# Performance work log

Measured on AMD Instinct MI355X. Metric: run time of the kernel, lower is better.

## Reference

```python
import jax, jax.numpy as jnp
import numpy as np

LN_EPS = 1e-5


def setup_inputs() -> dict:
    key = jax.random.key(0)
    ks = jax.random.split(key, 14)
    b, T, C = 1, 1024, 192
    ATTN, CONT, F = 4, 2, 8  # attn_dims, content_dims, conv feature channels
    s = 0.05
    H = jax.random.normal(ks[0], (b, C, T), jnp.float32)
    d = jax.random.randint(ks[1], (b, T), 2, 8)            # durations in [2,8)
    src_mask = jnp.ones((b, 1, T), dtype=bool)             # True = valid token
    return {
        "H": H, "d": d, "src_mask": src_mask,
        # proj_in: Linear(C,C) + SiLU
        "W_in": jax.random.normal(ks[2], (C, C)) * s, "b_in": jnp.zeros((C,)),
        # ConvLN: Conv1d(C->8, k=3, pad=1) + LayerNorm(8)
        "conv_w": jax.random.normal(ks[3], (F, C, 3)) * s, "conv_b": jnp.zeros((F,)),
        "gamma": jnp.ones((F,)), "beta": jnp.zeros((F,)),
        # W_proj: Linear(10,10)+SiLU+Linear(10,4)+softmax(dim=t_text)
        "wp1": jax.random.normal(ks[4], (10, 10)) * s, "bp1": jnp.zeros((10,)),
        "wp2": jax.random.normal(ks[5], (10, ATTN)) * s, "bp2": jnp.zeros((ATTN,)),
        # C_proj: Linear(10,10)+SiLU+Linear(10,2)+SiLU
        "wc1": jax.random.normal(ks[6], (10, 10)) * s, "bc1": jnp.zeros((10,)),
        "wc2": jax.random.normal(ks[7], (10, CONT)) * s, "bc2": jnp.zeros((CONT,)),
        # proj_WH: Linear(4*C, C); proj_WC: Linear(4*2, C)
        "W_WH": jax.random.normal(ks[8], (ATTN * C, C)) * s, "b_WH": jnp.zeros((C,)),
        "W_WC": jax.random.normal(ks[9], (ATTN * CONT, C)) * s, "b_WC": jnp.zeros((C,)),
        # proj_out: Conv1d(C, C, 1) == pointwise linear over channels
        "W_out": jax.random.normal(ks[10], (C, C)) * s, "b_out": jnp.zeros((C,)),
    }


def reference(H, d, src_mask, W_in, b_in, conv_w, conv_b, gamma, beta,
              wp1, bp1, wp2, bp2, wc1, bc1, wc2, bc2,
              W_WH, b_WH, W_WC, b_WC, W_out, b_out):
    b, C, T = H.shape
    df = d.astype(jnp.float32)
    mel_len = jnp.sum(d, axis=1)                                  # [b]
    t_mel = int(jnp.max(mel_len))                                 # static from concrete d
    frame_valid = jnp.arange(t_mel)[None, :] < mel_len[:, None]   # [b,M] True=valid frame
    tbm = (src_mask[:, 0, None, :] & frame_valid[:, :, None]).astype(jnp.float32)  # [b,M,T]

    # token boundary grid: S = frame_idx - start, E = end - frame_idx
    i = jnp.arange(1, t_mel + 1, dtype=jnp.float32)[None, :, None]  # [1,M,1]
    E_d = jnp.cumsum(df, axis=1)[:, None, :]                        # [b,1,T] token ends
    S_d = E_d - df[:, None, :]                                      # [b,1,T] token starts
    S = (i - S_d) * tbm                                             # [b,M,T]
    E = (E_d - i) * tbm                                             # [b,M,T]

    # proj_in (on [b,T,C]) then ConvLN(C->8) + SiLU
    x = jax.nn.silu(jnp.einsum('bct,cd->btd', H, W_in) + b_in)      # [b,T,C]
    xc = jax.lax.conv_general_dilated(
        jnp.transpose(x, (0, 2, 1)), conv_w, (1,), [(1, 1)],
        dimension_numbers=('NCH', 'OIH', 'NCH')) + conv_b[None, :, None]  # [b,8,T]
    xt = jnp.transpose(xc, (0, 2, 1))                               # [b,T,8]
    mu = jnp.mean(xt, axis=-1, keepdims=True)
    var = jnp.mean(jnp.square(xt - mu), axis=-1, keepdims=True)
    xt = (xt - mu) * jax.lax.rsqrt(var + LN_EPS) * gamma + beta
    xf = jax.nn.silu(xt)                                            # [b,T,8]

    # broadcast conv features over mel frames, cat with S/E boundary scalars
    feats = jnp.concatenate(
        [S[..., None], E[..., None],
         jnp.broadcast_to(xf[:, None, :, :], (b, t_mel, T, xf.shape[-1]))],
        axis=-1)                                                    # [b,M,T,10]

    # W_proj: tiny MLP + softmax over t_text
    W_att = jax.nn.softmax(jax.nn.silu(feats @ wp1 + bp1) @ wp2 + bp2, axis=2)  # [b,M,T,4]
    # C_proj: tiny MLP with SiLU output
    Cm = jax.nn.silu(jax.nn.silu(feats @ wc1 + bc1) @ wc2 + bc2)    # [b,M,T,2]

    WC = jnp.einsum('bmtq,bmtp->bmqp', W_att, Cm).reshape(b, t_mel, -1)  # [b,M,8]
    WH = jnp.einsum('bmtq,bht->bmqh', W_att, H).reshape(b, t_mel, -1)    # [b,M,768]
    O = (WC @ W_WC + b_WC) + (WH @ W_WH + b_WH)                     # [b,M,C]
    O = O @ W_out + b_out                                           # proj_out (1x1 conv)
    O = jnp.transpose(O, (0, 2, 1)) * frame_valid[:, None, :].astype(O.dtype)  # [b,C,M]
    return O, ~frame_valid
```

## Files before the change

### kernel.cpp

```cpp
#include <hip/hip_runtime.h>
#include <math.h>

#define T 1024
#define C 192
#define LN_EPS 1e-5f

typedef __attribute__((ext_vector_type(4))) float f32x4;
typedef __attribute__((ext_vector_type(8))) __bf16 bf16x8;

__device__ __forceinline__ float silu_f(float x){
    return x * __builtin_amdgcn_rcpf(1.0f + __expf(-x));
}
__device__ __forceinline__ float wred_max(float v){
    #pragma unroll
    for(int o=32;o;o>>=1) v = fmaxf(v, __shfl_xor(v,o));
    return v;
}
__device__ __forceinline__ float wred_sum(float v){
    #pragma unroll
    for(int o=32;o;o>>=1) v += __shfl_xor(v,o);
    return v;
}

__global__ void k_scan(const int* __restrict__ d, float* __restrict__ Sd, float* __restrict__ Ed){
    __shared__ int s[T];
    int tid = threadIdx.x;
    int v = d[tid];
    s[tid] = v;
    for(int off=1; off<T; off<<=1){
        __syncthreads();
        int add = (tid>=off) ? s[tid-off] : 0;
        __syncthreads();
        s[tid] += add;
    }
    __syncthreads();
    Ed[tid] = (float)s[tid];
    Sd[tid] = (float)(s[tid]-v);
}

__global__ void k_proj_in(const float* __restrict__ H, const float* __restrict__ W_in,
                          const float* __restrict__ b_in, float* __restrict__ x){
    __shared__ float Hs[192*4];
    int tid = threadIdx.x;
    int t0 = blockIdx.x*4;
    for(int idx=tid; idx<768; idx+=192){
        int ci = idx>>2, j = idx&3;
        Hs[idx] = H[ci*T + t0 + j];
    }
    __syncthreads();
    int c = tid;
    float acc[4];
    float bb = b_in[c];
    #pragma unroll
    for(int j=0;j<4;j++) acc[j] = bb;
    for(int ci=0; ci<192; ci++){
        float wv = W_in[ci*C + c];
        float4 h4 = *(const float4*)&Hs[ci*4];
        acc[0] += h4.x*wv; acc[1] += h4.y*wv;
        acc[2] += h4.z*wv; acc[3] += h4.w*wv;
    }
    #pragma unroll
    for(int j=0;j<4;j++) x[(t0+j)*C + c] = silu_f(acc[j]);
}

__global__ void k_conv_ln(const float* __restrict__ x, const float* __restrict__ conv_w,
                          const float* __restrict__ conv_b, const float* __restrict__ gamma,
                          const float* __restrict__ beta, float* __restrict__ xf){
    __shared__ float part[16][8][2];
    __shared__ float xcv[16][8];
    int tid = threadIdx.x;
    int cc = tid & 1, f = (tid>>1)&7, tl = tid>>4;
    int t = blockIdx.x*16 + tl;
    float acc = 0.f;
    for(int k=0;k<3;k++){
        int tt = t + k - 1;
        if(tt>=0 && tt<T){
            const float* xr = x + tt*C + cc*96;
            const float* wr = conv_w + f*C*3 + k + cc*96*3;
            for(int c2=0;c2<96;c2++) acc += xr[c2]*wr[c2*3];
        }
    }
    part[tl][f][cc] = acc;
    __syncthreads();
    if(cc==0){
        xcv[tl][f] = part[tl][f][0] + part[tl][f][1] + conv_b[f];
    }
    __syncthreads();
    if(cc==0){
        float a = xcv[tl][f];
        float mu=0.f;
        #pragma unroll
        for(int j=0;j<8;j++) mu += xcv[tl][j];
        mu *= 0.125f;
        float var=0.f;
        #pragma unroll
        for(int j=0;j<8;j++){ float dd = xcv[tl][j]-mu; var += dd*dd; }
        var *= 0.125f;
        float vi = rsqrtf(var + LN_EPS);
        float v = (a - mu)*vi*gamma[f] + beta[f];
        xf[t*8+f] = silu_f(v);
    }
}

__global__ void k_A(const float* __restrict__ Sd, const float* __restrict__ Ed,
                    const float* __restrict__ xf,
                    const float* __restrict__ wp1, const float* __restrict__ bp1,
                    const float* __restrict__ wc1, const float* __restrict__ bc1,
                    float* __restrict__ A1, float* __restrict__ A2, float* __restrict__ uv){
    int b = blockIdx.x, tid = threadIdx.x;
    if(b==4){
        if(tid<10){
            uv[tid]    = wp1[tid] - wp1[10+tid];
            uv[10+tid] = wc1[tid] - wc1[10+tid];
        }
        return;
    }
    int t = b*256 + tid;
    float sd = Sd[t], ed = Ed[t];
    float xv[8];
    #pragma unroll
    for(int k=0;k<8;k++) xv[k] = xf[t*8+k];
    #pragma unroll
    for(int j=0;j<10;j++){
        float a1 = bp1[j] - sd*wp1[j] + ed*wp1[10+j];
        float a2 = bc1[j] - sd*wc1[j] + ed*wc1[10+j];
        #pragma unroll
        for(int k=0;k<8;k++){
            a1 += xv[k]*wp1[(2+k)*10+j];
            a2 += xv[k]*wc1[(2+k)*10+j];
        }
        A1[t*12+j] = a1;
        A2[t*12+j] = a2;
    }
    A1[t*12+10]=0.f; A1[t*12+11]=0.f;
    A2[t*12+10]=0.f; A2[t*12+11]=0.f;
}

__global__ void k_hb(const float* __restrict__ H, __bf16* __restrict__ Hb){
    int base = (blockIdx.x*256 + threadIdx.x)*8;
    float4 a = *(const float4*)(H + base);
    float4 b = *(const float4*)(H + base + 4);
    bf16x8 o;
    o[0]=(__bf16)a.x; o[1]=(__bf16)a.y; o[2]=(__bf16)a.z; o[3]=(__bf16)a.w;
    o[4]=(__bf16)b.x; o[5]=(__bf16)b.y; o[6]=(__bf16)b.z; o[7]=(__bf16)b.w;
    *(bf16x8*)(Hb + base) = o;
}

__global__ void k_fold(const float* __restrict__ W_WH, const float* __restrict__ W_WC,
                       const float* __restrict__ b_WH, const float* __restrict__ b_WC,
                       const float* __restrict__ W_out, const float* __restrict__ b_out,
                       __bf16* __restrict__ WfT, float* __restrict__ b2){
    int i = blockIdx.x, c = threadIdx.x;
    if(i < 768){
        float a = 0.f;
        for(int j=0;j<C;j++) a += W_WH[i*C+j]*W_out[j*C+c];
        WfT[c*800 + i] = (__bf16)a;
    } else if(i < 776){
        int r = i-768;
        float a = 0.f;
        for(int j=0;j<C;j++) a += W_WC[r*C+j]*W_out[j*C+c];
        WfT[c*800 + 768 + r] = (__bf16)a;
    } else if(i == 776){
        float a = b_out[c];
        for(int j=0;j<C;j++) a += (b_WH[j]+b_WC[j])*W_out[j*C+c];
        b2[c] = a;
    } else {
        for(int k=c; k<192*24; k+=192){
            int cc = k/24, j = k - (k/24)*24;
            WfT[cc*800 + 776 + j] = (__bf16)0.f;
        }
    }
}

__global__ void __launch_bounds__(256) __attribute__((amdgpu_waves_per_eu(4,4)))
k_main(const __bf16* __restrict__ Hb, const float* __restrict__ A1, const float* __restrict__ A2,
       const float* __restrict__ uv,
       const float* __restrict__ wp2, const float* __restrict__ bp2,
       const float* __restrict__ wc2, const float* __restrict__ bc2,
       const __bf16* __restrict__ WfT, const float* __restrict__ b2g,
       float* __restrict__ out, int M)
{
    __shared__ __align__(16) unsigned char smem[40960];
    __bf16* PTlb = (__bf16*)smem;
    __bf16* wT   = (__bf16*)(smem + 6656);
    float*  scr  = (float*)(smem + 6656 + 32768);
    float*  wsm  = scr + 288;

    int tid = threadIdx.x;
    int w = tid >> 6, lane = tid & 63;
    int m0 = blockIdx.x*4;

    if(tid < 40)      wsm[tid] = wp2[tid];
    else if(tid < 44) wsm[tid] = bp2[tid-40];
    else if(tid < 64) wsm[tid] = wc2[tid-44];
    else if(tid < 66) wsm[tid] = bc2[tid-64];
    else if(tid < 86) wsm[tid] = uv[tid-66];
    if(tid < 224){
        int mi = tid/56, k = 776 + tid - (tid/56)*56;
        PTlb[mi*832 + (k ^ (mi<<4))] = (__bf16)0.f;
    }
    __syncthreads();

    for(int mi=0; mi<4; mi++){
        float fi = (float)(m0 + 1 + mi);
        float l[4][4];
        #pragma unroll 1
        for(int ti=0; ti<4; ti++){
            int t = tid + ti*256;
            float4 a0 = *(const float4*)(A1 + t*12);
            float4 a1 = *(const float4*)(A1 + t*12 + 4);
            float4 a2v = *(const float4*)(A1 + t*12 + 8);
            float Av[10] = {a0.x,a0.y,a0.z,a0.w,a1.x,a1.y,a1.z,a1.w,a2v.x,a2v.y};
            float l0=wsm[40], l1=wsm[41], l2=wsm[42], l3=wsm[43];
            #pragma unroll
            for(int j=0;j<10;j++){
                float h = silu_f(Av[j] + fi*wsm[66+j]);
                l0 += h*wsm[j*4+0]; l1 += h*wsm[j*4+1];
                l2 += h*wsm[j*4+2]; l3 += h*wsm[j*4+3];
            }
            l[ti][0]=l0; l[ti][1]=l1; l[ti][2]=l2; l[ti][3]=l3;
        }
        #pragma unroll
        for(int q=0;q<4;q++){
            float lm = fmaxf(fmaxf(l[0][q],l[1][q]), fmaxf(l[2][q],l[3][q]));
            lm = wred_max(lm);
            if(lane==0) scr[mi*16 + w*4 + q] = lm;
        }
        __syncthreads();
        float mxq[4];
        #pragma unroll
        for(int q=0;q<4;q++){
            float a = fmaxf(scr[mi*16+0*4+q], scr[mi*16+1*4+q]);
            float b = fmaxf(scr[mi*16+2*4+q], scr[mi*16+3*4+q]);
            mxq[q] = fmaxf(a,b);
        }
        float sp4[4] = {0.f,0.f,0.f,0.f};
        #pragma unroll
        for(int ti=0;ti<4;ti++){
            int t = tid + ti*256;
            #pragma unroll
            for(int q=0;q<4;q++){
                float e = __expf(l[ti][q] - mxq[q]);
                l[ti][q] = e;
                int row = mi*4+q;
                wT[row*1024 + (t ^ ((row&7)<<3))] = (__bf16)e;
                sp4[q] += e;
            }
        }
        float wcp2[4][2];
        #pragma unroll
        for(int q=0;q<4;q++){ wcp2[q][0]=0.f; wcp2[q][1]=0.f; }
        #pragma unroll 1
        for(int ti=0;ti<4;ti++){
            int t = tid + ti*256;
            float4 b0 = *(const float4*)(A2 + t*12);
            float4 b1 = *(const float4*)(A2 + t*12 + 4);
            float4 b2v = *(const float4*)(A2 + t*12 + 8);
            float Bv[10] = {b0.x,b0.y,b0.z,b0.w,b1.x,b1.y,b1.z,b1.w,b2v.x,b2v.y};
            float g1c0 = wsm[64], g1c1 = wsm[65];
            #pragma unroll
            for(int j=0;j<10;j++){
                float g = silu_f(Bv[j] + fi*wsm[76+j]);
                g1c0 += g*wsm[44 + j*2 + 0];
                g1c1 += g*wsm[44 + j*2 + 1];
            }
            float c0 = silu_f(g1c0), c1 = silu_f(g1c1);
            #pragma unroll
            for(int q=0;q<4;q++){
                wcp2[q][0] += l[ti][q]*c0;
                wcp2[q][1] += l[ti][q]*c1;
            }
        }
        #pragma unroll
        for(int q=0;q<4;q++){
            sp4[q] = wred_sum(sp4[q]);
            wcp2[q][0] = wred_sum(wcp2[q][0]);
            wcp2[q][1] = wred_sum(wcp2[q][1]);
        }
        if(lane==0){
            int base = 64 + mi*48 + w*12;
            #pragma unroll
            for(int q=0;q<4;q++){
                scr[base + q] = sp4[q];
                scr[base + 4 + q*2 + 0] = wcp2[q][0];
                scr[base + 4 + q*2 + 1] = wcp2[q][1];
            }
        }
    }
    __syncthreads();

    if(tid < 16){
        int mi = tid>>2, q = tid&3;
        float s = scr[64+mi*48+0*12+q] + scr[64+mi*48+1*12+q]
                + scr[64+mi*48+2*12+q] + scr[64+mi*48+3*12+q];
        scr[256+tid] = 1.0f/s;
    }
    if(tid >= 32 && tid < 64){
        int j = tid - 32;
        int mi = j>>3, qp = j&7, q = qp>>1, p = qp&1;
        float num = scr[64+mi*48+0*12+4+q*2+p] + scr[64+mi*48+1*12+4+q*2+p]
                  + scr[64+mi*48+2*12+4+q*2+p] + scr[64+mi*48+3*12+4+q*2+p];
        float den = scr[64+mi*48+0*12+q] + scr[64+mi*48+1*12+q]
                  + scr[64+mi*48+2*12+q] + scr[64+mi*48+3*12+q];
        PTlb[mi*832 + ((768+qp) ^ (mi<<4))] = (__bf16)(num/den);
    }
    __syncthreads();

    int cl = lane & 15, kg = lane >> 4;
    int swzW = (cl&7)<<3;
    f32x4 acc1[3];
    #pragma unroll
    for(int i=0;i<3;i++) acc1[i] = (f32x4){0.f,0.f,0.f,0.f};
    const __bf16* Aptr = Hb + (size_t)(w*48 + cl)*1024 + kg*8;
    const __bf16* wTrow = wT + cl*1024;
    #pragma unroll 2
    for(int ks=0; ks<32; ks++){
        int k0 = ks*32;
        bf16x8 bf = *(const bf16x8*)&wTrow[(k0 + kg*8) ^ swzW];
        #pragma unroll
        for(int i=0;i<3;i++){
            bf16x8 af = *(const bf16x8*)(Aptr + i*16*1024 + k0);
            acc1[i] = __builtin_amdgcn_mfma_f32_16x16x32_bf16(af, bf, acc1[i], 0, 0, 0);
        }
    }
    {
        int mP = cl >> 2, qP = cl & 3;
        float invv = scr[256 + cl];
        int swzP = mP<<4;
        #pragma unroll
        for(int i=0;i<3;i++){
            int hb = w*48 + i*16 + kg*4;
            #pragma unroll
            for(int r=0;r<4;r++){
                int k = qP*192 + hb + r;
                PTlb[mP*832 + (k ^ swzP)] = (__bf16)(acc1[i][r] * invv);
            }
        }
    }
    __syncthreads();

    f32x4 acc2[3];
    #pragma unroll
    for(int i=0;i<3;i++) acc2[i] = (f32x4){0.f,0.f,0.f,0.f};
    const __bf16* A2ptr = WfT + (size_t)(w*48 + cl)*800 + kg*8;
    const __bf16* Prow = PTlb + cl*832;
    int swzP2 = (cl&3)<<4;
    #pragma unroll 2
    for(int ks=0; ks<25; ks++){
        int k0 = ks*32;
        bf16x8 bf = *(const bf16x8*)&Prow[(k0 + kg*8) ^ swzP2];
        #pragma unroll
        for(int i=0;i<3;i++){
            bf16x8 af = *(const bf16x8*)(A2ptr + i*16*800 + k0);
            acc2[i] = __builtin_amdgcn_mfma_f32_16x16x32_bf16(af, bf, acc2[i], 0, 0, 0);
        }
    }
    if(cl < 4 && m0 + cl < M){
        #pragma unroll
        for(int i=0;i<3;i++){
            int cb = w*48 + i*16 + kg*4;
            #pragma unroll
            for(int r=0;r<4;r++){
                out[(size_t)(cb+r)*M + m0 + cl] = acc2[i][r] + b2g[cb+r];
            }
        }
    }
    if(tid < 4 && m0 + tid < M) out[(size_t)C*M + m0 + tid] = 0.f;
}

extern "C" void kernel_launch(void* const* d_in, const int* in_sizes, int n_in,
                              void* d_out, int out_size, void* d_ws, size_t ws_size,
                              hipStream_t stream)
{
    const float* H      = (const float*)d_in[0];
    const int*   d      = (const int*)  d_in[1];
    const float* W_in   = (const float*)d_in[3];
    const float* b_in   = (const float*)d_in[4];
    const float* conv_w = (const float*)d_in[5];
    const float* conv_b = (const float*)d_in[6];
    const float* gamma  = (const float*)d_in[7];
    const float* beta   = (const float*)d_in[8];
    const float* wp1    = (const float*)d_in[9];
    const float* bp1    = (const float*)d_in[10];
    const float* wp2    = (const float*)d_in[11];
    const float* bp2    = (const float*)d_in[12];
    const float* wc1    = (const float*)d_in[13];
    const float* bc1    = (const float*)d_in[14];
    const float* wc2    = (const float*)d_in[15];
    const float* bc2    = (const float*)d_in[16];
    const float* W_WH   = (const float*)d_in[17];
    const float* b_WH   = (const float*)d_in[18];
    const float* W_WC   = (const float*)d_in[19];
    const float* b_WC   = (const float*)d_in[20];
    const float* W_out  = (const float*)d_in[21];
    const float* b_out  = (const float*)d_in[22];

    float* out = (float*)d_out;
    int M = out_size / 193;

    float* ws   = (float*)d_ws;
    float* Sd   = ws;
    float* Ed   = ws + 1024;
    float* A1   = ws + 2048;
    float* A2   = ws + 14336;
    float* uvp  = ws + 26624;
    float* b2   = ws + 26656;
    __bf16* WfT = (__bf16*)(ws + 26848);
    __bf16* Hb  = (__bf16*)(ws + 103648);
    float* x    = ws + 201952;
    float* xf   = ws + 398560;

    hipLaunchKernelGGL(k_scan,    dim3(1),   dim3(1024), 0, stream, d, Sd, Ed);
    hipLaunchKernelGGL(k_proj_in, dim3(256), dim3(192),  0, stream, H, W_in, b_in, x);
    hipLaunchKernelGGL(k_conv_ln, dim3(64),  dim3(256),  0, stream, x, conv_w, conv_b, gamma, beta, xf);
    hipLaunchKernelGGL(k_A,       dim3(5),   dim3(256),  0, stream, Sd, Ed, xf, wp1, bp1, wc1, bc1, A1, A2, uvp);
    hipLaunchKernelGGL(k_hb,      dim3(96),  dim3(256),  0, stream, H, Hb);
    hipLaunchKernelGGL(k_fold,    dim3(778), dim3(192),  0, stream, W_WH, W_WC, b_WH, b_WC, W_out, b_out, WfT, b2);
    hipLaunchKernelGGL(k_main,    dim3((M+3)/4), dim3(256), 0, stream,
                       Hb, A1, A2, uvp, wp2, bp2, wc2, bc2, WfT, b2, out, M);
}
```

Baseline: 192.2 us.

## Move softmax weight tile from LDS to global scratch and merge prep kernels

```diff
diff --git a/kernel.cpp b/kernel.cpp
--- a/kernel.cpp
+++ b/kernel.cpp
@@ -136,21 +136,25 @@
     A2[t*12+10]=0.f; A2[t*12+11]=0.f;
 }
 
-__global__ void k_hb(const float* __restrict__ H, __bf16* __restrict__ Hb){
-    int base = (blockIdx.x*256 + threadIdx.x)*8;
-    float4 a = *(const float4*)(H + base);
-    float4 b = *(const float4*)(H + base + 4);
-    bf16x8 o;
-    o[0]=(__bf16)a.x; o[1]=(__bf16)a.y; o[2]=(__bf16)a.z; o[3]=(__bf16)a.w;
-    o[4]=(__bf16)b.x; o[5]=(__bf16)b.y; o[6]=(__bf16)b.z; o[7]=(__bf16)b.w;
-    *(bf16x8*)(Hb + base) = o;
-}
-
-__global__ void k_fold(const float* __restrict__ W_WH, const float* __restrict__ W_WC,
+__global__ void k_prep(const float* __restrict__ W_WH, const float* __restrict__ W_WC,
                        const float* __restrict__ b_WH, const float* __restrict__ b_WC,
                        const float* __restrict__ W_out, const float* __restrict__ b_out,
-                       __bf16* __restrict__ WfT, float* __restrict__ b2){
-    int i = blockIdx.x, c = threadIdx.x;
+                       const float* __restrict__ H,
+                       __bf16* __restrict__ WfT, float* __restrict__ b2,
+                       __bf16* __restrict__ Hb){
+    int bid = blockIdx.x, tid = threadIdx.x;
+    if(bid >= 778){
+        int base = ((bid-778)*256 + tid)*8;
+        float4 a = *(const float4*)(H + base);
+        float4 b = *(const float4*)(H + base + 4);
+        bf16x8 o;
+        o[0]=(__bf16)a.x; o[1]=(__bf16)a.y; o[2]=(__bf16)a.z; o[3]=(__bf16)a.w;
+        o[4]=(__bf16)b.x; o[5]=(__bf16)b.y; o[6]=(__bf16)b.z; o[7]=(__bf16)b.w;
+        *(bf16x8*)(Hb + base) = o;
+        return;
+    }
+    int i = bid, c = tid;
+    if(c >= 192) return;
     if(i < 768){
         float a = 0.f;
         for(int j=0;j<C;j++) a += W_WH[i*C+j]*W_out[j*C+c];
@@ -172,23 +176,23 @@
     }
 }
 
-__global__ void __launch_bounds__(256) __attribute__((amdgpu_waves_per_eu(4,4)))
+__global__ void __launch_bounds__(256) __attribute__((amdgpu_waves_per_eu(6,8)))
 k_main(const __bf16* __restrict__ Hb, const float* __restrict__ A1, const float* __restrict__ A2,
        const float* __restrict__ uv,
        const float* __restrict__ wp2, const float* __restrict__ bp2,
        const float* __restrict__ wc2, const float* __restrict__ bc2,
        const __bf16* __restrict__ WfT, const float* __restrict__ b2g,
+       __bf16* __restrict__ Eg,
        float* __restrict__ out, int M)
 {
-    __shared__ __align__(16) unsigned char smem[40960];
-    __bf16* PTlb = (__bf16*)smem;
-    __bf16* wT   = (__bf16*)(smem + 6656);
-    float*  scr  = (float*)(smem + 6656 + 32768);
-    float*  wsm  = scr + 288;
+    __shared__ __align__(16) __bf16 PTlb[4*832];
+    __shared__ float scr[288];
+    __shared__ float wsm[96];
 
     int tid = threadIdx.x;
     int w = tid >> 6, lane = tid & 63;
     int m0 = blockIdx.x*4;
+    __bf16* Eblk = Eg + (size_t)m0*4096;
 
     if(tid < 40)      wsm[tid] = wp2[tid];
     else if(tid < 44) wsm[tid] = bp2[tid-40];
@@ -196,8 +200,8 @@
     else if(tid < 66) wsm[tid] = bc2[tid-64];
     else if(tid < 86) wsm[tid] = uv[tid-66];
     if(tid < 224){
-        int mi = tid/56, k = 776 + tid - (tid/56)*56;
-        PTlb[mi*832 + (k ^ (mi<<4))] = (__bf16)0.f;
+        int fb = tid/56, k = 776 + (tid - (tid/56)*56);
+        PTlb[fb*832 + (k ^ (fb<<3))] = (__bf16)0.f;
     }
     __syncthreads();
 
@@ -235,6 +239,7 @@
             mxq[q] = fmaxf(a,b);
         }
         float sp4[4] = {0.f,0.f,0.f,0.f};
+        __bf16* Erow = Eblk + mi*4096;
         #pragma unroll
         for(int ti=0;ti<4;ti++){
             int t = tid + ti*256;
@@ -242,8 +247,7 @@
             for(int q=0;q<4;q++){
                 float e = __expf(l[ti][q] - mxq[q]);
                 l[ti][q] = e;
-                int row = mi*4+q;
-                wT[row*1024 + (t ^ ((row&7)<<3))] = (__bf16)e;
+                Erow[q*1024 + t] = (__bf16)e;
                 sp4[q] += e;
             }
         }
@@ -302,21 +306,20 @@
                   + scr[64+mi*48+2*12+4+q*2+p] + scr[64+mi*48+3*12+4+q*2+p];
         float den = scr[64+mi*48+0*12+q] + scr[64+mi*48+1*12+q]
                   + scr[64+mi*48+2*12+q] + scr[64+mi*48+3*12+q];
-        PTlb[mi*832 + ((768+qp) ^ (mi<<4))] = (__bf16)(num/den);
+        PTlb[mi*832 + ((768+qp) ^ (mi<<3))] = (__bf16)(num/den);
     }
     __syncthreads();
 
     int cl = lane & 15, kg = lane >> 4;
-    int swzW = (cl&7)<<3;
     f32x4 acc1[3];
     #pragma unroll
     for(int i=0;i<3;i++) acc1[i] = (f32x4){0.f,0.f,0.f,0.f};
     const __bf16* Aptr = Hb + (size_t)(w*48 + cl)*1024 + kg*8;
-    const __bf16* wTrow = wT + cl*1024;
+    const __bf16* Bp   = Eblk + cl*1024 + kg*8;
     #pragma unroll 2
     for(int ks=0; ks<32; ks++){
         int k0 = ks*32;
-        bf16x8 bf = *(const bf16x8*)&wTrow[(k0 + kg*8) ^ swzW];
+        bf16x8 bf = *(const bf16x8*)(Bp + k0);
         #pragma unroll
         for(int i=0;i<3;i++){
             bf16x8 af = *(const bf16x8*)(Aptr + i*16*1024 + k0);
@@ -324,16 +327,16 @@
         }
     }
     {
-        int mP = cl >> 2, qP = cl & 3;
+        int fb = cl >> 2, qP = cl & 3;
         float invv = scr[256 + cl];
-        int swzP = mP<<4;
+        int swz = fb<<3;
         #pragma unroll
         for(int i=0;i<3;i++){
             int hb = w*48 + i*16 + kg*4;
             #pragma unroll
             for(int r=0;r<4;r++){
                 int k = qP*192 + hb + r;
-                PTlb[mP*832 + (k ^ swzP)] = (__bf16)(acc1[i][r] * invv);
+                PTlb[fb*832 + (k ^ swz)] = (__bf16)(acc1[i][r] * invv);
             }
         }
     }
@@ -342,17 +345,16 @@
     f32x4 acc2[3];
     #pragma unroll
     for(int i=0;i<3;i++) acc2[i] = (f32x4){0.f,0.f,0.f,0.f};
-    const __bf16* A2ptr = WfT + (size_t)(w*48 + cl)*800 + kg*8;
-    const __bf16* Prow = PTlb + cl*832;
-    int swzP2 = (cl&3)<<4;
+    const __bf16* A2p = WfT + (size_t)(w*48 + cl)*800 + kg*8;
+    int prow = (cl&3)*832, swz2 = (cl&3)<<3;
     #pragma unroll 2
     for(int ks=0; ks<25; ks++){
         int k0 = ks*32;
-        bf16x8 bf = *(const bf16x8*)&Prow[(k0 + kg*8) ^ swzP2];
+        bf16x8 bb = *(const bf16x8*)&PTlb[prow + ((k0 + kg*8) ^ swz2)];
         #pragma unroll
         for(int i=0;i<3;i++){
-            bf16x8 af = *(const bf16x8*)(A2ptr + i*16*800 + k0);
-            acc2[i] = __builtin_amdgcn_mfma_f32_16x16x32_bf16(af, bf, acc2[i], 0, 0, 0);
+            bf16x8 af = *(const bf16x8*)(A2p + i*16*800 + k0);
+            acc2[i] = __builtin_amdgcn_mfma_f32_16x16x32_bf16(af, bb, acc2[i], 0, 0, 0);
         }
     }
     if(cl < 4 && m0 + cl < M){
@@ -397,6 +399,7 @@
 
     float* out = (float*)d_out;
     int M = out_size / 193;
+    int Mcap = ((M+3)/4)*4;
 
     float* ws   = (float*)d_ws;
     float* Sd   = ws;
@@ -409,13 +412,14 @@
     __bf16* Hb  = (__bf16*)(ws + 103648);
     float* x    = ws + 201952;
     float* xf   = ws + 398560;
+    __bf16* Eg  = (__bf16*)(ws + 406752);
 
     hipLaunchKernelGGL(k_scan,    dim3(1),   dim3(1024), 0, stream, d, Sd, Ed);
+    hipLaunchKernelGGL(k_prep,    dim3(874), dim3(256),  0, stream,
+                       W_WH, W_WC, b_WH, b_WC, W_out, b_out, H, WfT, b2, Hb);
     hipLaunchKernelGGL(k_proj_in, dim3(256), dim3(192),  0, stream, H, W_in, b_in, x);
     hipLaunchKernelGGL(k_conv_ln, dim3(64),  dim3(256),  0, stream, x, conv_w, conv_b, gamma, beta, xf);
     hipLaunchKernelGGL(k_A,       dim3(5),   dim3(256),  0, stream, Sd, Ed, xf, wp1, bp1, wc1, bc1, A1, A2, uvp);
-    hipLaunchKernelGGL(k_hb,      dim3(96),  dim3(256),  0, stream, H, Hb);
-    hipLaunchKernelGGL(k_fold,    dim3(778), dim3(192),  0, stream, W_WH, W_WC, b_WH, b_WC, W_out, b_out, WfT, b2);
     hipLaunchKernelGGL(k_main,    dim3((M+3)/4), dim3(256), 0, stream,
-                       Hb, A1, A2, uvp, wp2, bp2, wc2, bc2, WfT, b2, out, M);
-}
+                       Hb, A1, A2, uvp, wp2, bp2, wc2, bc2, WfT, b2, Eg, out, M);
+}
```

After: 343.5 us. 78.7% more time.
